# Kernel tuning notes

Hardware: AMD Instinct MI355X
Metric: run time of the kernel (lower is better)

The kernel has to match this reference:

```python
import jax, jax.numpy as jnp
import numpy as np
import math

CH_IN, MID, PS, DSTATE = 64, 128, 1024, 16
DTRANK = math.ceil(PS / 16)  # 64
B, H, W = 4, 256, 256


def conv2d(x, w, b=None, stride=1, pad=0, groups=1):
    out = jax.lax.conv_general_dilated(
        x, w, (stride, stride), [(pad, pad), (pad, pad)],
        feature_group_count=groups, dimension_numbers=('NCHW', 'OIHW', 'NCHW'))
    return out if b is None else out + b[None, :, None, None]


def groupnorm(x, g, b, ngroups=2, eps=1e-5):
    bb, c, hh, ww = x.shape
    xr = x.reshape(bb, ngroups, c // ngroups, hh, ww)
    mu = xr.mean(axis=(2, 3, 4), keepdims=True)
    var = xr.var(axis=(2, 3, 4), keepdims=True)
    xn = ((xr - mu) * jax.lax.rsqrt(var + eps)).reshape(bb, c, hh, ww)
    return xn * g[None, :, None, None] + b[None, :, None, None]


def silu(x):
    return x * jax.nn.sigmoid(x)


def selective_scan(u, delta, A, Bm, Cm, D):
    # u, delta: (b, l, d); A: (d, n); Bm, Cm: (b, l, n); D: (d,)
    dA = jnp.exp(jnp.einsum('bld,dn->bldn', delta, A))          # (b,l,d,n)
    dBu = (delta * u)[..., None] * Bm[:, :, None, :]             # (b,l,d,n)
    bsz, l, d = u.shape
    n = A.shape[1]

    def step(carry, inp):
        dA_i, dBu_i, C_i = inp                                   # (b,d,n),(b,d,n),(b,n)
        carry = dA_i * carry + dBu_i
        y = jnp.einsum('bdn,bn->bd', carry, C_i)
        return carry, y

    x0 = jnp.zeros((bsz, d, n), dtype=u.dtype)
    _, ys = jax.lax.scan(step, x0, (dA.transpose(1, 0, 2, 3), dBu.transpose(1, 0, 2, 3), Cm.transpose(1, 0, 2)))
    y = ys.transpose(1, 0, 2)                                    # (b,l,d)
    return y + u * D


def mamba_block(x, inproj_w, conv_w, conv_b, xproj_w, dtp_w, dtp_b, alog, dd):
    xr = conv2d(x, inproj_w, None, 1, 1, MID // 2)               # (b, 2*MID, h, w)
    xs, res = jnp.split(xr, 2, axis=1)
    xs = silu(conv2d(xs, conv_w, conv_b, 1, 0, MID // 2))
    b, c, h, w = xs.shape
    u = xs.reshape(b, c, h * w)                                  # (b, l=c, d=h*w)
    A = -jnp.exp(alog.astype(jnp.float32))                       # (d, n)
    x_dbl = jnp.einsum('bld,kd->blk', u, xproj_w)
    delta, Bm, Cm = jnp.split(x_dbl, [DTRANK, DTRANK + DSTATE], axis=-1)
    delta = jax.nn.softplus(jnp.einsum('blr,dr->bld', delta, dtp_w) + dtp_b)
    y = selective_scan(u, delta, A, Bm, Cm, dd.astype(jnp.float32))
    y = y.reshape(b, c, h, w)
    return y * silu(res)


def forward(x, w_in, b_in,
            gn0_g, gn0_b, inproj0_w, conv0_w, conv0_b, xproj0_w, dtp0_w, dtp0_b, alog0, dd0,
            gn1_g, gn1_b, inproj1_w, conv1_w, conv1_b, xproj1_w, dtp1_w, dtp1_b, alog1, dd1,
            w_out, b_out):
    h = conv2d(x, w_in, b_in, 8, 0, CH_IN // 2)                  # (B, MID, H/8, W/8)
    h = mamba_block(groupnorm(h, gn0_g, gn0_b), inproj0_w, conv0_w, conv0_b, xproj0_w, dtp0_w, dtp0_b, alog0, dd0) + h
    h = mamba_block(groupnorm(h, gn1_g, gn1_b), inproj1_w, conv1_w, conv1_b, xproj1_w, dtp1_w, dtp1_b, alog1, dd1) + h
    out = conv2d(h, w_out, b_out, 1, 0, CH_IN // 2)
    out = jax.image.resize(out, (out.shape[0], out.shape[1], out.shape[2] * 8, out.shape[3] * 8), method='bilinear')
    return out


def setup_inputs():
    key = jax.random.key(0)
    ks = jax.random.split(key, 16)
    def rn(k, shp, s=0.05):
        return s * jax.random.normal(k, shp, jnp.float32)
    alog = jnp.log(jnp.broadcast_to(jnp.arange(1, DSTATE + 1, dtype=jnp.float32), (PS, DSTATE)))
    inp = {
        'x': jax.random.normal(ks[0], (B, CH_IN, H, W), jnp.float32),
        'w_in': rn(ks[1], (MID, 2, 8, 8)), 'b_in': jnp.zeros((MID,), jnp.float32),
        'gn0_g': jnp.ones((MID,), jnp.float32), 'gn0_b': jnp.zeros((MID,), jnp.float32),
        'inproj0_w': rn(ks[2], (2 * MID, 2, 3, 3)),
        'conv0_w': rn(ks[3], (MID, 2, 1, 1)), 'conv0_b': jnp.zeros((MID,), jnp.float32),
        'xproj0_w': rn(ks[4], (DTRANK + 2 * DSTATE, PS), 0.02),
        'dtp0_w': rn(ks[5], (PS, DTRANK), 0.02), 'dtp0_b': rn(ks[6], (PS,), 0.02),
        'alog0': alog, 'dd0': jnp.ones((PS,), jnp.float32),
        'gn1_g': jnp.ones((MID,), jnp.float32), 'gn1_b': jnp.zeros((MID,), jnp.float32),
        'inproj1_w': rn(ks[7], (2 * MID, 2, 3, 3)),
        'conv1_w': rn(ks[8], (MID, 2, 1, 1)), 'conv1_b': jnp.zeros((MID,), jnp.float32),
        'xproj1_w': rn(ks[9], (DTRANK + 2 * DSTATE, PS), 0.02),
        'dtp1_w': rn(ks[10], (PS, DTRANK), 0.02), 'dtp1_b': rn(ks[11], (PS,), 0.02),
        'alog1': alog, 'dd1': jnp.ones((PS,), jnp.float32),
        'w_out': rn(ks[12], (MID, MID // (CH_IN // 2), 1, 1)), 'b_out': jnp.zeros((MID,), jnp.float32),
    }
    return inp


def reference(x, w_in, b_in,
              gn0_g, gn0_b, inproj0_w, conv0_w, conv0_b, xproj0_w, dtp0_w, dtp0_b, alog0, dd0,
              gn1_g, gn1_b, inproj1_w, conv1_w, conv1_b, xproj1_w, dtp1_w, dtp1_b, alog1, dd1,
              w_out, b_out):
    return forward(x, w_in, b_in,
                   gn0_g, gn0_b, inproj0_w, conv0_w, conv0_b, xproj0_w, dtp0_w, dtp0_b, alog0, dd0,
                   gn1_g, gn1_b, inproj1_w, conv1_w, conv1_b, xproj1_w, dtp1_w, dtp1_b, alog1, dd1,
                   w_out, b_out)
```

## Files before the change

### kernel.cpp

```cpp
#include <hip/hip_runtime.h>
#include <hip/hip_bf16.h>

#define BN 4
#define MID 128
#define P 1024
#define PS 1024
#define DSTATE 16
#define DTRANK 64
#define XD 96
#define HOUT 256

typedef __hip_bfloat16 bf16;

__device__ __forceinline__ float b2f(bf16 v) { return __bfloat162float(v); }
__device__ __forceinline__ float dload(const void* p, int i, bool isbf) {
  return isbf ? b2f(((const bf16*)p)[i]) : ((const float*)p)[i];
}
__device__ __forceinline__ float bfl(unsigned u) {
  union { unsigned i; float f; } c; c.i = u << 16; return c.f;
}
__device__ __forceinline__ float bfh(unsigned u) {
  union { unsigned i; float f; } c; c.i = u & 0xffff0000u; return c.f;
}

#define NPARAM 24
#define TOTAL_PARAMS 392192
#define CONV_PER_BLOCK 766
struct PtrPack { const void* p[NPARAM]; };

__device__ __forceinline__ void find_tensor(int dst, int& tt, int& off) {
  const int offs[NPARAM + 1] = {0,16384,16512,16640,16768,21376,21632,21760,120064,185600,
                                186624,203008,204032,204160,204288,208896,209152,209280,
                                307584,373120,374144,390528,391552,392064,392192};
  int t = 0, base = 0;
#pragma unroll
  for (int q = 1; q < NPARAM; ++q) {
    if (dst >= offs[q]) { t = q; base = offs[q]; }
  }
  tt = t; off = dst - base;
}

__global__ __launch_bounds__(256) void conv_in_kernel(
    const void* __restrict__ x, const unsigned* __restrict__ alog_raw,
    PtrPack pk, float* __restrict__ pp, float* __restrict__ h,
    float2* __restrict__ partA) {
  bool isbf = (alog_raw[0] != 0u);
  int blk = blockIdx.x, t = threadIdx.x;

  for (int i = t; i < CONV_PER_BLOCK; i += 256) {
    int dst = blk * CONV_PER_BLOCK + i;
    int tt, off;
    find_tensor(dst, tt, off);
    int src = off;
    if (tt == 7 || tt == 17) {
      int j = off & 3, q = off >> 2;
      int k = q % 96, d4 = q / 96;
      src = k * 1024 + d4 * 4 + j;
    } else if (tt == 8 || tt == 18) {
      src = (off & 1023) * 64 + (off >> 10);
    }
    pp[dst] = dload(pk.p[tt], src, isbf);
  }

  __shared__ float wlds[512];
  __shared__ float blds[4];
  __shared__ float ls[8];
  int tid = blk * 256 + t;
  int p = tid & 1023; int g = (tid >> 10) & 31; int b = tid >> 15;
  for (int q = t; q < 512; q += 256) {
    int i = q >> 8, kh = (q >> 5) & 7, j = (q >> 3) & 3, kw = q & 7;
    wlds[q] = dload(pk.p[0], (g * 4 + j) * 128 + i * 64 + kh * 8 + kw, isbf);
  }
  if (t < 4) blds[t] = dload(pk.p[1], g * 4 + t, isbf);
  __syncthreads();

  int oy = p >> 5, ox = p & 31;
  float acc0 = blds[0], acc1 = blds[1], acc2 = blds[2], acc3 = blds[3];
  if (isbf) {
    const uint4* xp = (const uint4*)x;
    size_t base = ((size_t)b * 64 + g * 2) * 8192;
    for (int i = 0; i < 2; ++i) {
      size_t cb = base + (size_t)i * 8192 + (size_t)oy * 256 + ox;
#pragma unroll
      for (int kh = 0; kh < 8; ++kh) {
        uint4 v = xp[cb + kh * 32];
        float xv[8] = {bfl(v.x),bfh(v.x),bfl(v.y),bfh(v.y),bfl(v.z),bfh(v.z),bfl(v.w),bfh(v.w)};
        const float* wk = &wlds[(i * 8 + kh) * 32];
#pragma unroll
        for (int kw = 0; kw < 8; ++kw) {
          float xvv = xv[kw];
          acc0 += xvv * wk[kw];
          acc1 += xvv * wk[8 + kw];
          acc2 += xvv * wk[16 + kw];
          acc3 += xvv * wk[24 + kw];
        }
      }
    }
  } else {
    const float4* xf = (const float4*)x;
    size_t base = ((size_t)b * 64 + g * 2) * 16384;
    for (int i = 0; i < 2; ++i) {
      size_t cb = base + (size_t)i * 16384 + (size_t)oy * 512 + ox * 2;
#pragma unroll
      for (int kh = 0; kh < 8; ++kh) {
        float4 v0 = xf[cb + kh * 64];
        float4 v1 = xf[cb + kh * 64 + 1];
        float xv[8] = {v0.x,v0.y,v0.z,v0.w,v1.x,v1.y,v1.z,v1.w};
        const float* wk = &wlds[(i * 8 + kh) * 32];
#pragma unroll
        for (int kw = 0; kw < 8; ++kw) {
          float xvv = xv[kw];
          acc0 += xvv * wk[kw];
          acc1 += xvv * wk[8 + kw];
          acc2 += xvv * wk[16 + kw];
          acc3 += xvv * wk[24 + kw];
        }
      }
    }
  }
  size_t ob = ((size_t)b * 128 + g * 4) * 1024 + p;
  h[ob] = acc0; h[ob + 1024] = acc1; h[ob + 2048] = acc2; h[ob + 3072] = acc3;

  float s  = acc0 + acc1 + acc2 + acc3;
  float s2 = acc0*acc0 + acc1*acc1 + acc2*acc2 + acc3*acc3;
#pragma unroll
  for (int off = 32; off > 0; off >>= 1) { s += __shfl_xor(s, off); s2 += __shfl_xor(s2, off); }
  int wid = t >> 6;
  if ((t & 63) == 0) { ls[wid * 2] = s; ls[wid * 2 + 1] = s2; }
  __syncthreads();
  if (t == 0)
    partA[blk] = make_float2(ls[0] + ls[2] + ls[4] + ls[6], ls[1] + ls[3] + ls[5] + ls[7]);
}

__global__ __launch_bounds__(256) void fused_u_kernel(
    const float* __restrict__ h, const float2* __restrict__ partial, int perB, int cnt,
    const float* __restrict__ gng, const float* __restrict__ gnb,
    const float* __restrict__ iw, const float* __restrict__ cw,
    const float* __restrict__ cb, float* __restrict__ u) {
  int blk = blockIdx.x;
  int h2 = blk & 1, g3 = (blk >> 1) & 31, b = blk >> 6;
  int ic0 = g3 * 2;
  __shared__ float tile[2][34][36];
  __shared__ float sred[2];
  if (threadIdx.x < 64) {
    float s = 0.f, s2 = 0.f;
    int base = b * perB;
    for (int i = threadIdx.x; i < cnt; i += 64) { float2 v = partial[base + i]; s += v.x; s2 += v.y; }
#pragma unroll
    for (int off = 32; off > 0; off >>= 1) { s += __shfl_xor(s, off); s2 += __shfl_xor(s2, off); }
    if (threadIdx.x == 0) { sred[0] = s; sred[1] = s2; }
  }
  for (int t = threadIdx.x; t < 2448; t += 256) ((float*)tile)[t] = 0.f;
  __syncthreads();
  float mu = sred[0] * (1.f / 65536.f);
  float var = sred[1] * (1.f / 65536.f) - mu * mu;
  float rs = rsqrtf(var + 1e-5f);
  float a0 = rs * gng[ic0],     o0 = gnb[ic0]     - mu * a0;
  float a1 = rs * gng[ic0 + 1], o1 = gnb[ic0 + 1] - mu * a1;
  const float* h0 = h + ((size_t)b * MID + ic0) * P;
  for (int t = threadIdx.x; t < 2048; t += 256) {
    int ch = t >> 10, px = t & 1023, y = px >> 5, xx = px & 31;
    float v = h0[ch * P + px];
    tile[ch][y + 1][xx + 1] = ch ? (v * a1 + o1) : (v * a0 + o0);
  }
  __syncthreads();
  const float* w0 = iw + (size_t)(4 * g3) * 18;
#pragma unroll
  for (int q = 0; q < 2; ++q) {
    int px = h2 * 512 + q * 256 + threadIdx.x;
    int y = px >> 5, xx = px & 31;
    float nb0[9], nb1[9];
#pragma unroll
    for (int ky = 0; ky < 3; ++ky)
#pragma unroll
      for (int kx = 0; kx < 3; ++kx) {
        nb0[ky * 3 + kx] = tile[0][y + ky][xx + kx];
        nb1[ky * 3 + kx] = tile[1][y + ky][xx + kx];
      }
    float xsv[4];
#pragma unroll
    for (int s4 = 0; s4 < 4; ++s4) {
      const float* wr = w0 + s4 * 18;
      float acc = 0.f;
#pragma unroll
      for (int k = 0; k < 9; ++k) acc += nb0[k] * wr[k] + nb1[k] * wr[9 + k];
      xsv[s4] = acc;
    }
#pragma unroll
    for (int j = 0; j < 4; ++j) {
      int c = 4 * g3 + j;
      int e4 = (j >> 1) * 2;
      float acc = cb[c] + cw[2 * c] * xsv[e4] + cw[2 * c + 1] * xsv[e4 + 1];
      u[((size_t)b * MID + c) * P + px] = acc / (1.f + __expf(-acc));
    }
  }
}

__global__ __launch_bounds__(256) void xdbl_delta_kernel(
    const float* __restrict__ u, const float* __restrict__ xwp,
    const float* __restrict__ dwt, const float* __restrict__ db,
    float* __restrict__ dlt_t, float* __restrict__ u_t, float* __restrict__ bct) {
  int bl = blockIdx.x;
  int b = bl >> 7, l = bl & 127;
  int t = threadIdx.x;
  __shared__ float4 us[256];
  __shared__ float4 accs[96];
  __shared__ float xds[64];
  const float4* up = (const float4*)(u + (size_t)bl * P);
  us[t] = up[t];
  __syncthreads();

  float4 acc = make_float4(0.f, 0.f, 0.f, 0.f);
  if (t < 192) {
    int s = (t >= 96) ? 1 : 0, k = t - s * 96;
    const float4* wp = (const float4*)xwp;
#pragma unroll 4
    for (int i = 0; i < 128; ++i) {
      int d4 = 2 * i + s;
      float4 w4 = wp[d4 * 96 + k];
      float4 u4 = us[d4];
      acc.x += u4.x * w4.x; acc.y += u4.y * w4.y; acc.z += u4.z * w4.z; acc.w += u4.w * w4.w;
    }
    if (s) accs[k] = acc;
  } else {
    float* ubase = u_t + ((size_t)b * 1024) * 128 + l;
    const float* usf = (const float*)us;
    for (int i = t - 192; i < 1024; i += 64) ubase[(size_t)i * 128] = usf[i];
  }
  __syncthreads();
  if (t < 96) {
    float4 o = accs[t];
    acc.x += o.x; acc.y += o.y; acc.z += o.z; acc.w += o.w;
    float v = (acc.x + acc.y) + (acc.z + acc.w);
    if (t < 64) xds[t] = v;
    else bct[((size_t)b * 32 + (t - 64)) * 128 + l] = v;
  }
  __syncthreads();

  float a0 = db[t], a1 = db[t + 256], a2 = db[t + 512], a3 = db[t + 768];
#pragma unroll 8
  for (int r = 0; r < 64; ++r) {
    float xr = xds[r];
    const float* wr = dwt + r * 1024 + t;
    a0 += xr * wr[0];
    a1 += xr * wr[256];
    a2 += xr * wr[512];
    a3 += xr * wr[768];
  }
  float* dbase = dlt_t + ((size_t)b * 1024) * 128 + l;
  float vals[4] = {a0, a1, a2, a3};
#pragma unroll
  for (int j = 0; j < 4; ++j) {
    float a = vals[j];
    float sp = fmaxf(a, 0.f) + log1pf(__expf(-fabsf(a)));
    dbase[(size_t)(t + 256 * j) * 128] = sp;
  }
}

__global__ __launch_bounds__(256) void scan_kernel(
    const float* __restrict__ u_t, const float* __restrict__ dlt_t,
    const float* __restrict__ bct, const float* __restrict__ alog,
    const float* __restrict__ dd, float* __restrict__ y_t) {
  int tid = blockIdx.x * 256 + threadIdx.x;
  int n = tid & 15; int d = (tid >> 4) & 1023; int b = tid >> 14;
  float A = -__expf(alog[d * DSTATE + n]);
  float D = dd[d];
  const float4* ut = (const float4*)(u_t   + ((size_t)b * 1024 + d) * 128);
  const float4* dt = (const float4*)(dlt_t + ((size_t)b * 1024 + d) * 128);
  const float4* Bt = (const float4*)(bct + ((size_t)b * 32 + n) * 128);
  const float4* Ct = (const float4*)(bct + ((size_t)b * 32 + 16 + n) * 128);
  float4* yp = (float4*)(y_t + ((size_t)b * 1024 + d) * 128);
  float state = 0.f;
#pragma unroll 2
  for (int lc = 0; lc < 32; ++lc) {
    float4 dl4 = dt[lc], u4 = ut[lc], B4 = Bt[lc], C4 = Ct[lc];
    float4 yo;
#define SSTEP(c) { float dA = __expf(dl4.c * A); state = dA * state + dl4.c * u4.c * B4.c; \
    float yv = state * C4.c; yv += __shfl_xor(yv, 1, 16); yv += __shfl_xor(yv, 2, 16); \
    yv += __shfl_xor(yv, 4, 16); yv += __shfl_xor(yv, 8, 16); yo.c = yv + u4.c * D; }
    SSTEP(x) SSTEP(y) SSTEP(z) SSTEP(w)
#undef SSTEP
    if (n == 0) yp[lc] = yo;
  }
}

__global__ __launch_bounds__(256) void merge_res_kernel(
    const float* __restrict__ hin, const float2* __restrict__ partial, int perB, int cnt,
    const float* __restrict__ gng, const float* __restrict__ gnb,
    const float* __restrict__ iw, const float* __restrict__ y_t,
    float* __restrict__ hout, float2* __restrict__ part_out) {
  int blk = blockIdx.x;
  int h2 = blk & 1, gq = (blk >> 1) & 31, b = blk >> 6;
  int g = 32 + gq;
  int ic0 = g * 2;
  __shared__ float tile[2][34][36];
  __shared__ float sred[2];
  __shared__ float ls[8];
  if (threadIdx.x < 64) {
    float s = 0.f, s2 = 0.f;
    int base = b * perB + cnt;
    for (int i = threadIdx.x; i < cnt; i += 64) { float2 v = partial[base + i]; s += v.x; s2 += v.y; }
#pragma unroll
    for (int off = 32; off > 0; off >>= 1) { s += __shfl_xor(s, off); s2 += __shfl_xor(s2, off); }
    if (threadIdx.x == 0) { sred[0] = s; sred[1] = s2; }
  }
  for (int t = threadIdx.x; t < 2448; t += 256) ((float*)tile)[t] = 0.f;
  __syncthreads();
  float mu = sred[0] * (1.f / 65536.f);
  float var = sred[1] * (1.f / 65536.f) - mu * mu;
  float rs = rsqrtf(var + 1e-5f);
  float a0 = rs * gng[ic0],     o0 = gnb[ic0]     - mu * a0;
  float a1 = rs * gng[ic0 + 1], o1 = gnb[ic0 + 1] - mu * a1;
  const float* h0 = hin + ((size_t)b * MID + ic0) * P;
  for (int t = threadIdx.x; t < 2048; t += 256) {
    int ch = t >> 10, px = t & 1023, y = px >> 5, xx = px & 31;
    float v = h0[ch * P + px];
    tile[ch][y + 1][xx + 1] = ch ? (v * a1 + o1) : (v * a0 + o0);
  }
  __syncthreads();
  const float* w0 = iw + (size_t)(4 * g) * 18;
  float sacc = 0.f, s2acc = 0.f;
#pragma unroll
  for (int q = 0; q < 2; ++q) {
    int px = h2 * 512 + q * 256 + threadIdx.x;
    int y = px >> 5, xx = px & 31;
    float nb0[9], nb1[9];
#pragma unroll
    for (int ky = 0; ky < 3; ++ky)
#pragma unroll
      for (int kx = 0; kx < 3; ++kx) {
        nb0[ky * 3 + kx] = tile[0][y + ky][xx + kx];
        nb1[ky * 3 + kx] = tile[1][y + ky][xx + kx];
      }
    float4 yv4 = *(const float4*)(y_t + ((size_t)b * 1024 + px) * 128 + gq * 4);
    float yv[4] = {yv4.x, yv4.y, yv4.z, yv4.w};
#pragma unroll
    for (int j = 0; j < 4; ++j) {
      const float* wr = w0 + j * 18;
      float res = 0.f;
#pragma unroll
      for (int k = 0; k < 9; ++k) res += nb0[k] * wr[k] + nb1[k] * wr[9 + k];
      int c = 4 * gq + j;
      size_t oi = ((size_t)b * MID + c) * P + px;
      float s = res / (1.f + __expf(-res));
      float val = yv[j] * s + hin[oi];
      hout[oi] = val;
      sacc += val; s2acc += val * val;
    }
  }
  if (part_out) {
#pragma unroll
    for (int off = 32; off > 0; off >>= 1) { sacc += __shfl_xor(sacc, off); s2acc += __shfl_xor(s2acc, off); }
    int wid = threadIdx.x >> 6;
    if ((threadIdx.x & 63) == 0) { ls[wid * 2] = sacc; ls[wid * 2 + 1] = s2acc; }
    __syncthreads();
    if (threadIdx.x == 0)
      part_out[blk] = make_float2(ls[0] + ls[2] + ls[4] + ls[6], ls[1] + ls[3] + ls[5] + ls[7]);
  }
}

__global__ __launch_bounds__(256) void out_kernel(
    const float* __restrict__ h, const float* __restrict__ w, const float* __restrict__ bias,
    const unsigned* __restrict__ alog_raw, void* __restrict__ out) {
  int bc = blockIdx.x;
  int c = bc & 127, b = bc >> 7;
  int t = threadIdx.x;
  __shared__ float cop[1024];
  __shared__ float txs[256];
  __shared__ int x0s[256], x1s[256];
  {
    float cx = ((float)t + 0.5f) * 0.125f - 0.5f;
    int ix0 = (int)floorf(cx);
    txs[t] = cx - (float)ix0;
    x0s[t] = max(ix0, 0);
    x1s[t] = min(ix0 + 1, 31);
  }
  const float* hp = h + ((size_t)b * MID + (c & ~3)) * P;
  float w0 = w[c * 4], w1 = w[c * 4 + 1], w2 = w[c * 4 + 2], w3 = w[c * 4 + 3];
  float bo = bias[c];
  {
    const float4* h4 = (const float4*)hp;
    float4 v0 = h4[t], v1 = h4[256 + t], v2 = h4[512 + t], v3 = h4[768 + t];
    float4 a;
    a.x = bo + w0 * v0.x + w1 * v1.x + w2 * v2.x + w3 * v3.x;
    a.y = bo + w0 * v0.y + w1 * v1.y + w2 * v2.y + w3 * v3.y;
    a.z = bo + w0 * v0.z + w1 * v1.z + w2 * v2.z + w3 * v3.z;
    a.w = bo + w0 * v0.w + w1 * v1.w + w2 * v2.w + w3 * v3.w;
    ((float4*)cop)[t] = a;
  }
  __syncthreads();
  bool isbf = (alog_raw[0] != 0u);
  size_t obase = (size_t)bc * 16384;
  for (int gidx = t; gidx < 16384; gidx += 256) {
    int ox4 = gidx & 63, oy = gidx >> 6;
    float ty = txs[oy]; int y0 = x0s[oy], y1 = x1s[oy];
    const float* r0 = cop + y0 * 32;
    const float* r1 = cop + y1 * 32;
    float v[4];
#pragma unroll
    for (int j = 0; j < 4; ++j) {
      int ox = ox4 * 4 + j;
      float tx = txs[ox]; int xx0 = x0s[ox], xx1 = x1s[ox];
      float v00 = r0[xx0], v01 = r0[xx1], v10 = r1[xx0], v11 = r1[xx1];
      v[j] = (1.f - ty) * ((1.f - tx) * v00 + tx * v01) + ty * ((1.f - tx) * v10 + tx * v11);
    }
    if (isbf) {
      ushort4 s;
      s.x = __hip_bfloat16_raw(__float2bfloat16(v[0])).x;
      s.y = __hip_bfloat16_raw(__float2bfloat16(v[1])).x;
      s.z = __hip_bfloat16_raw(__float2bfloat16(v[2])).x;
      s.w = __hip_bfloat16_raw(__float2bfloat16(v[3])).x;
      ((ushort4*)out)[obase + gidx] = s;
    } else {
      ((float4*)out)[obase + gidx] = make_float4(v[0], v[1], v[2], v[3]);
    }
  }
}

extern "C" void kernel_launch(void* const* d_in, const int* in_sizes, int n_in,
                              void* d_out, int out_size, void* d_ws, size_t ws_size,
                              hipStream_t stream) {
  const void* x = d_in[0];
  const unsigned* alog_raw = (const unsigned*)d_in[11];

  PtrPack pk;
  for (int i = 0; i < NPARAM; ++i) pk.p[i] = d_in[i + 1];

  float* ws = (float*)d_ws;
  float* pp    = ws;
  float* h0    = pp + TOTAL_PARAMS;
  float* h1    = h0 + 524288;
  float* u     = h1 + 524288;
  float* u_t   = u + 524288;
  float* dlt_t = u_t + 524288;
  float* y_t   = dlt_t + 524288;
  float* bct   = y_t + 524288;
  float* partA = bct + 16384;
  float* partB = partA + 1024;

  const float* w_out = pp + 391552;
  const float* b_out = pp + 392064;
  const float* gn_g[2], *gn_b[2], *inproj_w[2], *conv_w[2], *conv_b[2],
             *xproj_w[2], *dtp_w[2], *dtp_b[2], *alog_f[2], *dd_f[2];
  for (int k = 0; k < 2; ++k) {
    const float* base = pp + 16512 + (size_t)k * 187520;
    gn_g[k] = base + 0;       gn_b[k] = base + 128;
    inproj_w[k] = base + 256; conv_w[k] = base + 4864;
    conv_b[k] = base + 5120;  xproj_w[k] = base + 5248;
    dtp_w[k] = base + 103552; dtp_b[k] = base + 169088;
    alog_f[k] = base + 170112; dd_f[k] = base + 186496;
  }

  conv_in_kernel<<<512, 256, 0, stream>>>(x, alog_raw, pk, pp, h0, (float2*)partA);

  float* hbuf[2] = { h0, h1 };
  const float2* partIn = (const float2*)partA;
  int perB = 128, cnt = 64;
  for (int blk = 0; blk < 2; ++blk) {
    float* hin  = hbuf[blk & 1];
    float* hout = hbuf[(blk + 1) & 1];
    fused_u_kernel<<<256, 256, 0, stream>>>(hin, partIn, perB, cnt, gn_g[blk], gn_b[blk],
                                            inproj_w[blk], conv_w[blk], conv_b[blk], u);
    xdbl_delta_kernel<<<512, 256, 0, stream>>>(u, xproj_w[blk], dtp_w[blk], dtp_b[blk],
                                               dlt_t, u_t, bct);
    scan_kernel<<<256, 256, 0, stream>>>(u_t, dlt_t, bct, alog_f[blk], dd_f[blk], y_t);
    merge_res_kernel<<<256, 256, 0, stream>>>(hin, partIn, perB, cnt, gn_g[blk], gn_b[blk],
                                              inproj_w[blk], y_t, hout,
                                              blk == 0 ? (float2*)partB : nullptr);
    partIn = (const float2*)partB; perB = 64; cnt = 32;
  }

  out_kernel<<<512, 256, 0, stream>>>(h0, w_out, b_out, alog_raw, d_out);
}
```

Baseline: 355.6 us.

## Fuse u-conv with x-proj/delta and scan with residual merge per block

Merges the u-producing conv kernel with the x_dbl/delta projection kernel so u stays in shared memory. Each block now handles four sequence positions, which reuses the projection weights four times. The scan is also merged with the residual gate/merge kernel, so y is kept in shared memory instead of a global y_t buffer. This cuts the kernels per Mamba block from four to two and removes two intermediate global round-trips. In exchange, blocks use more shared memory and registers, the two s-halves recompute the full x-projection, and the merge stage's partial-statistics indexing changes.

Measured after the change: 362.3 us. Within noise of the previous version (+1.9%).

```diff
diff --git a/kernel.cpp b/kernel.cpp
--- a/kernel.cpp
+++ b/kernel.cpp
@@ -21,6 +21,9 @@
 }
 __device__ __forceinline__ float bfh(unsigned u) {
   union { unsigned i; float f; } c; c.i = u & 0xffff0000u; return c.f;
+}
+__device__ __forceinline__ float softplusf(float a) {
+  return fmaxf(a, 0.f) + log1pf(__expf(-fabsf(a)));
 }
 
 #define NPARAM 24
@@ -129,45 +132,53 @@
   if ((t & 63) == 0) { ls[wid * 2] = s; ls[wid * 2 + 1] = s2; }
   __syncthreads();
   if (t == 0)
-    partA[blk] = make_float2(ls[0] + ls[2] + ls[4] + ls[6], ls[1] + ls[3] + ls[5] + ls[7]);
-}
-
-__global__ __launch_bounds__(256) void fused_u_kernel(
-    const float* __restrict__ h, const float2* __restrict__ partial, int perB, int cnt,
+    partA[blk] = make_float2(ls[0] + ls[2] + ls[4] + ls[6],
+                             ls[1] + ls[3] + ls[5] + ls[7]);
+}
+
+__global__ __launch_bounds__(256) void fuse_u_xdbl_kernel(
+    const float* __restrict__ hin, const float2* __restrict__ part, int poff, int pstride,
     const float* __restrict__ gng, const float* __restrict__ gnb,
-    const float* __restrict__ iw, const float* __restrict__ cw,
-    const float* __restrict__ cb, float* __restrict__ u) {
-  int blk = blockIdx.x;
-  int h2 = blk & 1, g3 = (blk >> 1) & 31, b = blk >> 6;
+    const float* __restrict__ iw, const float* __restrict__ cw, const float* __restrict__ cb,
+    const float* __restrict__ xwp, const float* __restrict__ dwt, const float* __restrict__ db,
+    float* __restrict__ u_t, float* __restrict__ dlt_t, float* __restrict__ bct) {
+  int bid = blockIdx.x;
+  int s = bid & 1, g3 = (bid >> 1) & 31, b = bid >> 6;
+  int t = threadIdx.x;
   int ic0 = g3 * 2;
   __shared__ float tile[2][34][36];
+  __shared__ float4 us4[4][256];
+  __shared__ float4 accs4[96];
+  __shared__ float xds[4][64];
   __shared__ float sred[2];
-  if (threadIdx.x < 64) {
-    float s = 0.f, s2 = 0.f;
-    int base = b * perB;
-    for (int i = threadIdx.x; i < cnt; i += 64) { float2 v = partial[base + i]; s += v.x; s2 += v.y; }
-#pragma unroll
-    for (int off = 32; off > 0; off >>= 1) { s += __shfl_xor(s, off); s2 += __shfl_xor(s2, off); }
-    if (threadIdx.x == 0) { sred[0] = s; sred[1] = s2; }
-  }
-  for (int t = threadIdx.x; t < 2448; t += 256) ((float*)tile)[t] = 0.f;
+
+  if (t < 64) {
+    float2 v = part[b * 128 + poff + t * pstride];
+    float ss = v.x, s2 = v.y;
+#pragma unroll
+    for (int off = 32; off > 0; off >>= 1) { ss += __shfl_xor(ss, off); s2 += __shfl_xor(s2, off); }
+    if (t == 0) { sred[0] = ss; sred[1] = s2; }
+  }
+  for (int q = t; q < 2448; q += 256) ((float*)tile)[q] = 0.f;
   __syncthreads();
   float mu = sred[0] * (1.f / 65536.f);
   float var = sred[1] * (1.f / 65536.f) - mu * mu;
   float rs = rsqrtf(var + 1e-5f);
   float a0 = rs * gng[ic0],     o0 = gnb[ic0]     - mu * a0;
   float a1 = rs * gng[ic0 + 1], o1 = gnb[ic0 + 1] - mu * a1;
-  const float* h0 = h + ((size_t)b * MID + ic0) * P;
-  for (int t = threadIdx.x; t < 2048; t += 256) {
-    int ch = t >> 10, px = t & 1023, y = px >> 5, xx = px & 31;
+  const float* h0 = hin + ((size_t)b * MID + ic0) * P;
+  for (int q = t; q < 2048; q += 256) {
+    int ch = q >> 10, px = q & 1023, y = px >> 5, xx = px & 31;
     float v = h0[ch * P + px];
     tile[ch][y + 1][xx + 1] = ch ? (v * a1 + o1) : (v * a0 + o0);
   }
   __syncthreads();
+
   const float* w0 = iw + (size_t)(4 * g3) * 18;
-#pragma unroll
-  for (int q = 0; q < 2; ++q) {
-    int px = h2 * 512 + q * 256 + threadIdx.x;
+  float* usf = (float*)us4;
+#pragma unroll
+  for (int q = 0; q < 4; ++q) {
+    int px = q * 256 + t;
     int y = px >> 5, xx = px & 31;
     float nb0[9], nb1[9];
 #pragma unroll
@@ -191,85 +202,102 @@
       int c = 4 * g3 + j;
       int e4 = (j >> 1) * 2;
       float acc = cb[c] + cw[2 * c] * xsv[e4] + cw[2 * c + 1] * xsv[e4 + 1];
-      u[((size_t)b * MID + c) * P + px] = acc / (1.f + __expf(-acc));
-    }
-  }
-}
-
-__global__ __launch_bounds__(256) void xdbl_delta_kernel(
-    const float* __restrict__ u, const float* __restrict__ xwp,
-    const float* __restrict__ dwt, const float* __restrict__ db,
-    float* __restrict__ dlt_t, float* __restrict__ u_t, float* __restrict__ bct) {
-  int bl = blockIdx.x;
-  int b = bl >> 7, l = bl & 127;
-  int t = threadIdx.x;
-  __shared__ float4 us[256];
-  __shared__ float4 accs[96];
-  __shared__ float xds[64];
-  const float4* up = (const float4*)(u + (size_t)bl * P);
-  us[t] = up[t];
-  __syncthreads();
-
-  float4 acc = make_float4(0.f, 0.f, 0.f, 0.f);
+      usf[j * 1024 + px] = acc / (1.f + __expf(-acc));
+    }
+  }
+  __syncthreads();
+
+  float a0_ = 0.f, a1_ = 0.f, a2_ = 0.f, a3_ = 0.f;
   if (t < 192) {
-    int s = (t >= 96) ? 1 : 0, k = t - s * 96;
+    int kh = (t >= 96) ? 1 : 0, k = t - 96 * kh;
     const float4* wp = (const float4*)xwp;
 #pragma unroll 4
     for (int i = 0; i < 128; ++i) {
-      int d4 = 2 * i + s;
+      int d4 = 2 * i + kh;
       float4 w4 = wp[d4 * 96 + k];
-      float4 u4 = us[d4];
-      acc.x += u4.x * w4.x; acc.y += u4.y * w4.y; acc.z += u4.z * w4.z; acc.w += u4.w * w4.w;
-    }
-    if (s) accs[k] = acc;
-  } else {
-    float* ubase = u_t + ((size_t)b * 1024) * 128 + l;
-    const float* usf = (const float*)us;
-    for (int i = t - 192; i < 1024; i += 64) ubase[(size_t)i * 128] = usf[i];
+      float4 u0 = us4[0][d4], u1 = us4[1][d4], u2 = us4[2][d4], u3 = us4[3][d4];
+      a0_ += u0.x * w4.x + u0.y * w4.y + u0.z * w4.z + u0.w * w4.w;
+      a1_ += u1.x * w4.x + u1.y * w4.y + u1.z * w4.z + u1.w * w4.w;
+      a2_ += u2.x * w4.x + u2.y * w4.y + u2.z * w4.z + u2.w * w4.w;
+      a3_ += u3.x * w4.x + u3.y * w4.y + u3.z * w4.z + u3.w * w4.w;
+    }
+    if (kh) accs4[k] = make_float4(a0_, a1_, a2_, a3_);
+  } else if (s == 0) {
+    for (int i = t - 192; i < 1024; i += 64) {
+      float4 uv = make_float4(usf[i], usf[1024 + i], usf[2048 + i], usf[3072 + i]);
+      *(float4*)(u_t + ((size_t)b * 1024 + i) * 128 + 4 * g3) = uv;
+    }
   }
   __syncthreads();
   if (t < 96) {
-    float4 o = accs[t];
-    acc.x += o.x; acc.y += o.y; acc.z += o.z; acc.w += o.w;
-    float v = (acc.x + acc.y) + (acc.z + acc.w);
-    if (t < 64) xds[t] = v;
-    else bct[((size_t)b * 32 + (t - 64)) * 128 + l] = v;
-  }
-  __syncthreads();
-
-  float a0 = db[t], a1 = db[t + 256], a2 = db[t + 512], a3 = db[t + 768];
+    float4 o = accs4[t];
+    float v0 = a0_ + o.x, v1 = a1_ + o.y, v2 = a2_ + o.z, v3 = a3_ + o.w;
+    if (t < 64) {
+      xds[0][t] = v0; xds[1][t] = v1; xds[2][t] = v2; xds[3][t] = v3;
+    } else if (s == 0) {
+      *(float4*)(bct + ((size_t)b * 32 + (t - 64)) * 128 + 4 * g3) = make_float4(v0, v1, v2, v3);
+    }
+  }
+  __syncthreads();
+
+  int d0 = 512 * s + t, d1 = d0 + 256;
+  float bias0 = db[d0], bias1 = db[d1];
+  float acc00 = bias0, acc01 = bias0, acc02 = bias0, acc03 = bias0;
+  float acc10 = bias1, acc11 = bias1, acc12 = bias1, acc13 = bias1;
 #pragma unroll 8
   for (int r = 0; r < 64; ++r) {
-    float xr = xds[r];
-    const float* wr = dwt + r * 1024 + t;
-    a0 += xr * wr[0];
-    a1 += xr * wr[256];
-    a2 += xr * wr[512];
-    a3 += xr * wr[768];
-  }
-  float* dbase = dlt_t + ((size_t)b * 1024) * 128 + l;
-  float vals[4] = {a0, a1, a2, a3};
-#pragma unroll
-  for (int j = 0; j < 4; ++j) {
-    float a = vals[j];
-    float sp = fmaxf(a, 0.f) + log1pf(__expf(-fabsf(a)));
-    dbase[(size_t)(t + 256 * j) * 128] = sp;
-  }
-}
-
-__global__ __launch_bounds__(256) void scan_kernel(
-    const float* __restrict__ u_t, const float* __restrict__ dlt_t,
-    const float* __restrict__ bct, const float* __restrict__ alog,
-    const float* __restrict__ dd, float* __restrict__ y_t) {
-  int tid = blockIdx.x * 256 + threadIdx.x;
-  int n = tid & 15; int d = (tid >> 4) & 1023; int b = tid >> 14;
+    float x0 = xds[0][r], x1 = xds[1][r], x2 = xds[2][r], x3 = xds[3][r];
+    const float* wr = dwt + r * 1024 + 512 * s + t;
+    float w0_ = wr[0], w1_ = wr[256];
+    acc00 += x0 * w0_; acc01 += x1 * w0_; acc02 += x2 * w0_; acc03 += x3 * w0_;
+    acc10 += x0 * w1_; acc11 += x1 * w1_; acc12 += x2 * w1_; acc13 += x3 * w1_;
+  }
+  *(float4*)(dlt_t + ((size_t)b * 1024 + d0) * 128 + 4 * g3) =
+      make_float4(softplusf(acc00), softplusf(acc01), softplusf(acc02), softplusf(acc03));
+  *(float4*)(dlt_t + ((size_t)b * 1024 + d1) * 128 + 4 * g3) =
+      make_float4(softplusf(acc10), softplusf(acc11), softplusf(acc12), softplusf(acc13));
+}
+
+__global__ __launch_bounds__(256) void scan_merge_kernel(
+    const float* __restrict__ hin, const float2* __restrict__ part, int poff, int pstride,
+    const float* __restrict__ gng, const float* __restrict__ gnb, const float* __restrict__ iw,
+    const float* __restrict__ u_t, const float* __restrict__ dlt_t, const float* __restrict__ bct,
+    const float* __restrict__ alog, const float* __restrict__ dd_,
+    float* __restrict__ hout, float2* __restrict__ part_out) {
+  int bid = blockIdx.x;
+  int q = bid & 63, b = bid >> 6;
+  int t = threadIdx.x;
+  int n = t & 15, dl = t >> 4;
+  int d = q * 16 + dl;
+  __shared__ float y_s[16][132];
+  __shared__ float hs[64][3][18];
+  __shared__ float a_s[64], o_s[64];
+  __shared__ float sred[2];
+  __shared__ float ls[8];
+
+  if (t < 64) {
+    float2 v = part[b * 128 + poff + t * pstride];
+    float ss = v.x, s2 = v.y;
+#pragma unroll
+    for (int off = 32; off > 0; off >>= 1) { ss += __shfl_xor(ss, off); s2 += __shfl_xor(s2, off); }
+    if (t == 0) { sred[0] = ss; sred[1] = s2; }
+  }
+  __syncthreads();
+  float mu = sred[0] * (1.f / 65536.f);
+  float var = sred[1] * (1.f / 65536.f) - mu * mu;
+  float rs = rsqrtf(var + 1e-5f);
+  if (t < 64) {
+    float aa = rs * gng[64 + t];
+    a_s[t] = aa;
+    o_s[t] = gnb[64 + t] - mu * aa;
+  }
+
   float A = -__expf(alog[d * DSTATE + n]);
-  float D = dd[d];
+  float D = dd_[d];
   const float4* ut = (const float4*)(u_t   + ((size_t)b * 1024 + d) * 128);
   const float4* dt = (const float4*)(dlt_t + ((size_t)b * 1024 + d) * 128);
   const float4* Bt = (const float4*)(bct + ((size_t)b * 32 + n) * 128);
   const float4* Ct = (const float4*)(bct + ((size_t)b * 32 + 16 + n) * 128);
-  float4* yp = (float4*)(y_t + ((size_t)b * 1024 + d) * 128);
   float state = 0.f;
 #pragma unroll 2
   for (int lc = 0; lc < 32; ++lc) {
@@ -280,82 +308,53 @@
     yv += __shfl_xor(yv, 4, 16); yv += __shfl_xor(yv, 8, 16); yo.c = yv + u4.c * D; }
     SSTEP(x) SSTEP(y) SSTEP(z) SSTEP(w)
 #undef SSTEP
-    if (n == 0) yp[lc] = yo;
-  }
-}
-
-__global__ __launch_bounds__(256) void merge_res_kernel(
-    const float* __restrict__ hin, const float2* __restrict__ partial, int perB, int cnt,
-    const float* __restrict__ gng, const float* __restrict__ gnb,
-    const float* __restrict__ iw, const float* __restrict__ y_t,
-    float* __restrict__ hout, float2* __restrict__ part_out) {
-  int blk = blockIdx.x;
-  int h2 = blk & 1, gq = (blk >> 1) & 31, b = blk >> 6;
-  int g = 32 + gq;
-  int ic0 = g * 2;
-  __shared__ float tile[2][34][36];
-  __shared__ float sred[2];
-  __shared__ float ls[8];
-  if (threadIdx.x < 64) {
-    float s = 0.f, s2 = 0.f;
-    int base = b * perB + cnt;
-    for (int i = threadIdx.x; i < cnt; i += 64) { float2 v = partial[base + i]; s += v.x; s2 += v.y; }
-#pragma unroll
-    for (int off = 32; off > 0; off >>= 1) { s += __shfl_xor(s, off); s2 += __shfl_xor(s2, off); }
-    if (threadIdx.x == 0) { sred[0] = s; sred[1] = s2; }
-  }
-  for (int t = threadIdx.x; t < 2448; t += 256) ((float*)tile)[t] = 0.f;
-  __syncthreads();
-  float mu = sred[0] * (1.f / 65536.f);
-  float var = sred[1] * (1.f / 65536.f) - mu * mu;
-  float rs = rsqrtf(var + 1e-5f);
-  float a0 = rs * gng[ic0],     o0 = gnb[ic0]     - mu * a0;
-  float a1 = rs * gng[ic0 + 1], o1 = gnb[ic0 + 1] - mu * a1;
-  const float* h0 = hin + ((size_t)b * MID + ic0) * P;
-  for (int t = threadIdx.x; t < 2048; t += 256) {
-    int ch = t >> 10, px = t & 1023, y = px >> 5, xx = px & 31;
-    float v = h0[ch * P + px];
-    tile[ch][y + 1][xx + 1] = ch ? (v * a1 + o1) : (v * a0 + o0);
-  }
-  __syncthreads();
-  const float* w0 = iw + (size_t)(4 * g) * 18;
+    if (n == 0) *(float4*)&y_s[dl][4 * lc] = yo;
+  }
+  __syncthreads();
+
+  int py = q >> 1, px0 = (q & 1) * 16;
+  for (int m = t; m < 3456; m += 256) {
+    int ch = m / 54, rem = m - ch * 54;
+    int rr = rem / 18, cc = rem - rr * 18;
+    int gy = py - 1 + rr, gx = px0 - 1 + cc;
+    float v = 0.f;
+    if ((unsigned)gy < 32u && (unsigned)gx < 32u)
+      v = a_s[ch] * hin[((size_t)b * 128 + 64 + ch) * 1024 + gy * 32 + gx] + o_s[ch];
+    hs[ch][rr][cc] = v;
+  }
+  __syncthreads();
+
+  int px = t & 15, cg = t >> 4;
+  int gx_ = px0 + px;
   float sacc = 0.f, s2acc = 0.f;
 #pragma unroll
-  for (int q = 0; q < 2; ++q) {
-    int px = h2 * 512 + q * 256 + threadIdx.x;
-    int y = px >> 5, xx = px & 31;
-    float nb0[9], nb1[9];
+  for (int j = 0; j < 8; ++j) {
+    int c = cg * 8 + j;
+    int gq = c >> 2;
+    const float* wr = iw + (size_t)(4 * (32 + gq) + (c & 3)) * 18;
+    int ci = 2 * gq;
+    float res = 0.f;
 #pragma unroll
     for (int ky = 0; ky < 3; ++ky)
 #pragma unroll
-      for (int kx = 0; kx < 3; ++kx) {
-        nb0[ky * 3 + kx] = tile[0][y + ky][xx + kx];
-        nb1[ky * 3 + kx] = tile[1][y + ky][xx + kx];
-      }
-    float4 yv4 = *(const float4*)(y_t + ((size_t)b * 1024 + px) * 128 + gq * 4);
-    float yv[4] = {yv4.x, yv4.y, yv4.z, yv4.w};
-#pragma unroll
-    for (int j = 0; j < 4; ++j) {
-      const float* wr = w0 + j * 18;
-      float res = 0.f;
-#pragma unroll
-      for (int k = 0; k < 9; ++k) res += nb0[k] * wr[k] + nb1[k] * wr[9 + k];
-      int c = 4 * gq + j;
-      size_t oi = ((size_t)b * MID + c) * P + px;
-      float s = res / (1.f + __expf(-res));
-      float val = yv[j] * s + hin[oi];
-      hout[oi] = val;
-      sacc += val; s2acc += val * val;
-    }
+      for (int kx = 0; kx < 3; ++kx)
+        res += hs[ci][ky][px + kx] * wr[ky * 3 + kx] + hs[ci + 1][ky][px + kx] * wr[9 + ky * 3 + kx];
+    float sl = res / (1.f + __expf(-res));
+    size_t oi = ((size_t)b * 128 + c) * 1024 + py * 32 + gx_;
+    float val = y_s[px][c] * sl + hin[oi];
+    hout[oi] = val;
+    sacc += val; s2acc += val * val;
   }
   if (part_out) {
 #pragma unroll
     for (int off = 32; off > 0; off >>= 1) { sacc += __shfl_xor(sacc, off); s2acc += __shfl_xor(s2acc, off); }
-    int wid = threadIdx.x >> 6;
-    if ((threadIdx.x & 63) == 0) { ls[wid * 2] = sacc; ls[wid * 2 + 1] = s2acc; }
+    int wid = t >> 6;
+    if ((t & 63) == 0) { ls[wid * 2] = sacc; ls[wid * 2 + 1] = s2acc; }
     __syncthreads();
-    if (threadIdx.x == 0)
-      part_out[blk] = make_float2(ls[0] + ls[2] + ls[4] + ls[6], ls[1] + ls[3] + ls[5] + ls[7]);
+    if (t == 0) {
+      part_out[bid * 2]     = make_float2(ls[0] + ls[2], ls[1] + ls[3]);
+      part_out[bid * 2 + 1] = make_float2(ls[4] + ls[6], ls[5] + ls[7]);
+    }
   }
 }
 
@@ -430,44 +429,37 @@
   float* pp    = ws;
   float* h0    = pp + TOTAL_PARAMS;
   float* h1    = h0 + 524288;
-  float* u     = h1 + 524288;
-  float* u_t   = u + 524288;
+  float* u_t   = h1 + 524288;
   float* dlt_t = u_t + 524288;
-  float* y_t   = dlt_t + 524288;
-  float* bct   = y_t + 524288;
+  float* bct   = dlt_t + 524288;
   float* partA = bct + 16384;
   float* partB = partA + 1024;
 
   const float* w_out = pp + 391552;
   const float* b_out = pp + 392064;
-  const float* gn_g[2], *gn_b[2], *inproj_w[2], *conv_w[2], *conv_b[2],
-             *xproj_w[2], *dtp_w[2], *dtp_b[2], *alog_f[2], *dd_f[2];
-  for (int k = 0; k < 2; ++k) {
-    const float* base = pp + 16512 + (size_t)k * 187520;
-    gn_g[k] = base + 0;       gn_b[k] = base + 128;
-    inproj_w[k] = base + 256; conv_w[k] = base + 4864;
-    conv_b[k] = base + 5120;  xproj_w[k] = base + 5248;
-    dtp_w[k] = base + 103552; dtp_b[k] = base + 169088;
-    alog_f[k] = base + 170112; dd_f[k] = base + 186496;
-  }
 
   conv_in_kernel<<<512, 256, 0, stream>>>(x, alog_raw, pk, pp, h0, (float2*)partA);
 
   float* hbuf[2] = { h0, h1 };
-  const float2* partIn = (const float2*)partA;
-  int perB = 128, cnt = 64;
   for (int blk = 0; blk < 2; ++blk) {
+    const float* base = pp + 16512 + (size_t)blk * 187520;
+    const float* gng = base, *gnb = base + 128, *iw = base + 256;
+    const float* cw = base + 4864, *cb = base + 5120;
+    const float* xwp = base + 5248, *dwt = base + 103552, *db = base + 169088;
+    const float* alog = base + 170112, *dd = base + 186496;
     float* hin  = hbuf[blk & 1];
     float* hout = hbuf[(blk + 1) & 1];
-    fused_u_kernel<<<256, 256, 0, stream>>>(hin, partIn, perB, cnt, gn_g[blk], gn_b[blk],
-                                            inproj_w[blk], conv_w[blk], conv_b[blk], u);
-    xdbl_delta_kernel<<<512, 256, 0, stream>>>(u, xproj_w[blk], dtp_w[blk], dtp_b[blk],
-                                               dlt_t, u_t, bct);
-    scan_kernel<<<256, 256, 0, stream>>>(u_t, dlt_t, bct, alog_f[blk], dd_f[blk], y_t);
-    merge_res_kernel<<<256, 256, 0, stream>>>(hin, partIn, perB, cnt, gn_g[blk], gn_b[blk],
-                                              inproj_w[blk], y_t, hout,
-                                              blk == 0 ? (float2*)partB : nullptr);
-    partIn = (const float2*)partB; perB = 64; cnt = 32;
+    const float2* pIn = (const float2*)(blk ? partB : partA);
+    int pstr = blk ? 2 : 1;
+    int poffU = 0;
+    int poffM = blk ? 1 : 64;
+
+    fuse_u_xdbl_kernel<<<256, 256, 0, stream>>>(hin, pIn, poffU, pstr, gng, gnb,
+                                                iw, cw, cb, xwp, dwt, db,
+                                                u_t, dlt_t, bct);
+    scan_merge_kernel<<<256, 256, 0, stream>>>(hin, pIn, poffM, pstr, gng, gnb, iw,
+                                               u_t, dlt_t, bct, alog, dd, hout,
+                                               blk == 0 ? (float2*)partB : nullptr);
   }
 
   out_kernel<<<512, 256, 0, stream>>>(h0, w_out, b_out, alog_raw, d_out);
```
